# Performance work log

Hardware: AMD Instinct MI355X
Metric: run time of the kernel (lower is better)

Reference implementation:

```python
import jax, jax.numpy as jnp
import numpy as np

# Static hierarchical-sampling layout (hop-sorted prefixes), matching setup_inputs.
C0, C1, C2 = 50_000, 150_000, 300_000   # cumulative node counts for hops 0,1,2
E0, E1 = 300_000, 600_000               # per-edge-type edge counts for hop masks 0,1
T = 3                                    # number of hetero edge types
CIN, HID = 64, 128
LN_EPS = 1e-5
L2_EPS = 1e-12


def _seg_mean(msg, dst, n):
    # PyG scatter-mean: zero for isolated dst nodes
    s = jax.ops.segment_sum(msg, dst, num_segments=n)
    cnt = jax.ops.segment_sum(jnp.ones((dst.shape[0], 1), msg.dtype), dst, num_segments=n)
    return s / jnp.maximum(cnt, 1.0)


def _layer_norm(x, g, b):
    mu = jnp.mean(x, axis=-1, keepdims=True)
    var = jnp.var(x, axis=-1, keepdims=True)
    return (x - mu) * jax.lax.rsqrt(var + LN_EPS) * g + b


def setup_inputs() -> dict:
    key = jax.random.key(0)
    ks = jax.random.split(key, 16)
    x = jax.random.normal(ks[0], (C2, CIN), jnp.float32)
    eis = []
    for t in range(T):
        k1, k2, k3, k4 = jax.random.split(ks[1 + t], 4)
        src0 = jax.random.randint(k1, (E0,), 0, C1, jnp.int32)
        dst0 = jax.random.randint(k2, (E0,), 0, C0, jnp.int32)
        src1 = jax.random.randint(k3, (E1,), 0, C2, jnp.int32)
        dst1 = jax.random.randint(k4, (E1,), 0, C1, jnp.int32)
        eis.append(jnp.stack([jnp.concatenate([src0, src1]),
                              jnp.concatenate([dst0, dst1])]))
    s = 0.05
    Wp = jax.random.normal(ks[4], (T, CIN, CIN), jnp.float32) * s
    bp = jnp.zeros((T, CIN), jnp.float32)
    Wl = jax.random.normal(ks[5], (T, CIN, HID), jnp.float32) * s
    bl = jnp.zeros((T, HID), jnp.float32)
    Wr = jax.random.normal(ks[6], (T, CIN, HID), jnp.float32) * s
    Wl2 = jax.random.normal(ks[7], (T, HID, HID), jnp.float32) * s
    bl2 = jnp.zeros((T, HID), jnp.float32)
    Wr2 = jax.random.normal(ks[8], (T, HID, HID), jnp.float32) * s
    nm_node = jnp.concatenate([jnp.zeros(C0, jnp.int32),
                               jnp.ones(C1 - C0, jnp.int32),
                               jnp.full((C2 - C1,), 2, jnp.int32)])
    nm_edge = jnp.tile(jnp.concatenate([jnp.zeros(E0, jnp.int32),
                                        jnp.ones(E1, jnp.int32)]), T)
    return {"x": x, "ei0": eis[0], "ei1": eis[1], "ei2": eis[2],
            "nm_node": nm_node, "nm_edge": nm_edge,
            "Wp": Wp, "bp": bp, "Wl": Wl, "bl": bl, "Wr": Wr,
            "Wl2": Wl2, "bl2": bl2, "Wr2": Wr2,
            "g0": jnp.ones(HID, jnp.float32), "b0": jnp.zeros(HID, jnp.float32),
            "g1": jnp.ones(HID, jnp.float32), "b1": jnp.zeros(HID, jnp.float32)}


def reference(x, ei0, ei1, ei2, nm_node, nm_edge,
              Wp, bp, Wl, bl, Wr, Wl2, bl2, Wr2, g0, b0, g1, b1):
    eis = (ei0, ei1, ei2)
    # ---- conv 0: SAGEConv(project=True, normalize=True), full graph (trim layer=3) ----
    outs = []
    for t in range(T):
        src, dst = eis[t][0], eis[t][1]
        xp = jax.nn.relu(x @ Wp[t] + bp[t])           # project src features [C2, CIN]
        agg = _seg_mean(xp[src], dst, C2)             # mean over in-neighbors
        o = agg @ Wl[t] + bl[t] + x @ Wr[t]           # lin_l(agg)+bias + lin_r(root)
        o = o / jnp.maximum(jnp.linalg.norm(o, axis=-1, keepdims=True), L2_EPS)
        outs.append(o)
    h = jnp.mean(jnp.stack(outs, 0), 0)               # HeteroConv aggr='mean'
    h = _layer_norm(jax.nn.relu(h), g0, b0)           # relu -> LayerNorm (dropout=eval)
    # ---- conv 1: trim to layer=2 (node prefix C1, hop-0 edges only) ----
    h1 = h[:C1]
    outs = []
    for t in range(T):
        src, dst = eis[t][0, :E0], eis[t][1, :E0]
        agg = _seg_mean(h1[src], dst, C1)
        outs.append(agg @ Wl2[t] + bl2[t] + h1 @ Wr2[t])
    h2 = jnp.mean(jnp.stack(outs, 0), 0)
    h2 = _layer_norm(jax.nn.relu(h2), g1, b1)
    # ---- final trim to layer=1: seed nodes only ----
    return h2[:C0]
```

## Files before the change

### kernel.cpp

```cpp
#include <hip/hip_runtime.h>

#define C0n 50000
#define C1n 150000
#define C2n 300000
#define E0n 300000
#define E1n 600000
#define NEn (E0n + E1n)
#define PAD64 76
#define PAD128 140

typedef float  v4f    __attribute__((ext_vector_type(4)));
typedef float  v2f    __attribute__((ext_vector_type(2)));
typedef float  f32x4  __attribute__((ext_vector_type(4)));
typedef short  bf16x8 __attribute__((ext_vector_type(8)));
typedef unsigned short u16;

__device__ __forceinline__ u16 f2bf(float f){
    unsigned u = __builtin_bit_cast(unsigned, f);
    u += 0x7FFFu + ((u >> 16) & 1u);
    return (u16)(u >> 16);
}
__device__ __forceinline__ float bf2f(u16 h){
    unsigned u = ((unsigned)h) << 16;
    return __builtin_bit_cast(float, u);
}
__device__ __forceinline__ f32x4 mfma16(bf16x8 a, bf16x8 b, f32x4 c){
    return __builtin_amdgcn_mfma_f32_16x16x32_bf16(a, b, c, 0, 0, 0);
}
__device__ __forceinline__ float red16(float v){
    v += __shfl_xor(v, 1); v += __shfl_xor(v, 2);
    v += __shfl_xor(v, 4); v += __shfl_xor(v, 8);
    return v;
}
__device__ __forceinline__ bf16x8 frag8(const float* __restrict__ p){
    v4f a = *(const v4f*)p, b = *(const v4f*)(p + 4);
    bf16x8 r;
    r[0] = (short)f2bf(a[0]); r[1] = (short)f2bf(a[1]);
    r[2] = (short)f2bf(a[2]); r[3] = (short)f2bf(a[3]);
    r[4] = (short)f2bf(b[0]); r[5] = (short)f2bf(b[1]);
    r[6] = (short)f2bf(b[2]); r[7] = (short)f2bf(b[3]);
    return r;
}

__global__ __launch_bounds__(256) void k_wconv(const float* __restrict__ Wp,
    const float* __restrict__ Wl, const float* __restrict__ Wr,
    const float* __restrict__ Wl2, const float* __restrict__ Wr2,
    u16* __restrict__ Wp_c, u16* __restrict__ W1_c, u16* __restrict__ W2_c)
{
    const int i0 = blockIdx.x * 256 + threadIdx.x;
    const int stride = gridDim.x * 256;
    for (int idx = i0; idx < 3 * 64 * PAD64; idx += stride) {
        int t = idx / (64 * PAD64), r = idx % (64 * PAD64);
        int c = r / PAD64, k = r % PAD64;
        Wp_c[idx] = (k < 64) ? f2bf(Wp[t * 4096 + k * 64 + c]) : (u16)0;
    }
    for (int idx = i0; idx < 3 * 128 * PAD128; idx += stride) {
        int t = idx / (128 * PAD128), r = idx % (128 * PAD128);
        int c = r / PAD128, k = r % PAD128;
        u16 v = 0;
        if (k < 64)       v = f2bf(Wl[t * 8192 + k * 128 + c]);
        else if (k < 128) v = f2bf(Wr[t * 8192 + (k - 64) * 128 + c]);
        W1_c[idx] = v;
    }
    for (int idx = i0; idx < 6 * 128 * PAD128; idx += stride) {
        int m = idx / (128 * PAD128), r = idx % (128 * PAD128);
        int t = m % 3;
        const float* W = (m >= 3) ? Wr2 : Wl2;
        int c = r / PAD128, k = r % PAD128;
        W2_c[idx] = (k < 128) ? f2bf(W[t * 16384 + k * 128 + c]) : (u16)0;
    }
}

__global__ __launch_bounds__(256) void k_projm3(const float* __restrict__ x,
    const u16* __restrict__ Wp_c, const float* __restrict__ bp,
    u16* __restrict__ xp3)
{
    __shared__ __align__(16) u16 Wt[3 * 64 * PAD64];
    __shared__ float bps[3 * 64];
    const int tid = threadIdx.x;
    for (int i = tid; i < 192; i += 256) bps[i] = bp[i];
    for (int i = tid; i < 3 * 64 * PAD64 / 8; i += 256)
        ((bf16x8*)Wt)[i] = ((const bf16x8*)Wp_c)[i];
    __syncthreads();

    const int lane = tid & 63, wid = tid >> 6;
    const int lr = lane & 15, lg = lane >> 4;
    const int ntiles = C2n / 16;
    int rt = blockIdx.x * 4 + wid;
    const bool valid = (rt < ntiles);
    if (rt > ntiles - 1) rt = ntiles - 1;
    const int r0 = rt * 16;

    bf16x8 xa[2];
    xa[0] = frag8(&x[(size_t)(r0 + lr) * 64 + 0  + 8 * lg]);
    xa[1] = frag8(&x[(size_t)(r0 + lr) * 64 + 32 + 8 * lg]);

    for (int t = 0; t < 3; t++) {
        f32x4 acc[4];
#pragma unroll
        for (int n = 0; n < 4; n++) acc[n] = 0;
#pragma unroll
        for (int ks = 0; ks < 2; ks++) {
#pragma unroll
            for (int n = 0; n < 4; n++) {
                bf16x8 b = *(const bf16x8*)&Wt[t * 64 * PAD64 + (16 * n + lr) * PAD64 + ks * 32 + 8 * lg];
                acc[n] = mfma16(xa[ks], b, acc[n]);
            }
        }
        if (valid) {
            u16* xp = xp3 + (size_t)t * C2n * 64;
#pragma unroll
            for (int n = 0; n < 4; n++) {
                const float bb = bps[t * 64 + 16 * n + lr];
#pragma unroll
                for (int j = 0; j < 4; j++)
                    xp[(size_t)(r0 + 4 * lg + j) * 64 + 16 * n + lr] =
                        f2bf(fmaxf(acc[n][j] + bb, 0.f));
            }
        }
    }
}

__global__ __launch_bounds__(256) void k_hist(const int* __restrict__ d0,
    const int* __restrict__ d1, const int* __restrict__ d2,
    int* __restrict__ deg, int nE, int nV)
{
    const int e = blockIdx.x * 256 + threadIdx.x;
    if (e >= nE) return;
    const int y = blockIdx.y;
    const int* d = (y == 0) ? d0 : (y == 1) ? d1 : d2;
    atomicAdd(&deg[(size_t)y * nV + d[e]], 1);
}

__global__ __launch_bounds__(256) void k_scan_a(int* __restrict__ a, int n,
    int* __restrict__ bsum, int nblk)
{
    __shared__ int sd[256];
    const int t = threadIdx.x, y = blockIdx.y;
    int* arr = a + (size_t)y * n;
    const int base = blockIdx.x * 2048 + t * 8;
    int v[8];
#pragma unroll
    for (int j = 0; j < 8; j++) v[j] = (base + j < n) ? arr[base + j] : 0;
    int tot = 0;
#pragma unroll
    for (int j = 0; j < 8; j++) { int tmp = v[j]; v[j] = tot; tot += tmp; }
    sd[t] = tot; __syncthreads();
    for (int off = 1; off < 256; off <<= 1) {
        int xv = (t >= off) ? sd[t - off] : 0;
        __syncthreads();
        sd[t] += xv;
        __syncthreads();
    }
    const int excl = sd[t] - tot;
#pragma unroll
    for (int j = 0; j < 8; j++)
        if (base + j < n) arr[base + j] = excl + v[j];
    if (t == 255) bsum[y * nblk + blockIdx.x] = sd[255];
}

__global__ __launch_bounds__(256) void k_scan_b(int* __restrict__ bsum, int nblk)
{
    __shared__ int sd[256];
    const int t = threadIdx.x, y = blockIdx.y;
    int val = (t < nblk) ? bsum[y * nblk + t] : 0;
    sd[t] = val; __syncthreads();
    for (int off = 1; off < 256; off <<= 1) {
        int xv = (t >= off) ? sd[t - off] : 0;
        __syncthreads();
        sd[t] += xv;
        __syncthreads();
    }
    if (t < nblk) bsum[y * nblk + t] = sd[t] - val;
}

__global__ __launch_bounds__(256) void k_scan_c(int* __restrict__ a, int n,
    const int* __restrict__ bsum, int nblk)
{
    const int t = threadIdx.x, y = blockIdx.y;
    int* arr = a + (size_t)y * n;
    const int base = blockIdx.x * 2048 + t * 8;
    const int add = bsum[y * nblk + blockIdx.x];
#pragma unroll
    for (int j = 0; j < 8; j++)
        if (base + j < n) arr[base + j] += add;
}

__global__ __launch_bounds__(256) void k_fill(const int* __restrict__ s0,
    const int* __restrict__ s1, const int* __restrict__ s2,
    const int* __restrict__ d0, const int* __restrict__ d1, const int* __restrict__ d2,
    const int* __restrict__ rp, int* __restrict__ fill, int* __restrict__ el,
    int nE, int nV)
{
    const int e = blockIdx.x * 256 + threadIdx.x;
    if (e >= nE) return;
    const int y = blockIdx.y;
    const int* s = (y == 0) ? s0 : (y == 1) ? s1 : s2;
    const int* d = (y == 0) ? d0 : (y == 1) ? d1 : d2;
    const int dd = d[e];
    const int pos = rp[(size_t)y * nV + dd] + atomicAdd(&fill[(size_t)y * nV + dd], 1);
    el[(size_t)y * nE + pos] = s[e];
}

__global__ __launch_bounds__(256) void k_gath1(const int* __restrict__ rp1,
    const int* __restrict__ el1, const u16* __restrict__ xp3,
    u16* __restrict__ agg3)
{
    const int t = blockIdx.y;
    const int* rp = rp1 + (size_t)t * C1n;
    const int* el = el1 + (size_t)t * NEn;
    const u16* xp = xp3 + (size_t)t * C2n * 64;
    u16* aggt = agg3 + (size_t)t * C1n * 64;

    const int gid = blockIdx.x * 4 + (threadIdx.x >> 6);
    if (gid >= C1n) return;
    const int half = (threadIdx.x >> 5) & 1, l32 = threadIdx.x & 31;
    const int b = rp[gid];
    const int e = (gid == C1n - 1) ? NEn : rp[gid + 1];

    float s0 = 0.f, s1 = 0.f;
    int i = b + half;
    for (; i + 2 < e; i += 4) {
        const int sr0 = el[i], sr1 = el[i + 2];
        unsigned u0 = *(const unsigned*)&xp[(size_t)sr0 * 64 + l32 * 2];
        unsigned u1 = *(const unsigned*)&xp[(size_t)sr1 * 64 + l32 * 2];
        s0 += bf2f((u16)(u0 & 0xffffu)) + bf2f((u16)(u1 & 0xffffu));
        s1 += bf2f((u16)(u0 >> 16)) + bf2f((u16)(u1 >> 16));
    }
    for (; i < e; i += 2) {
        const int sr = el[i];
        unsigned u = *(const unsigned*)&xp[(size_t)sr * 64 + l32 * 2];
        s0 += bf2f((u16)(u & 0xffffu));
        s1 += bf2f((u16)(u >> 16));
    }
    s0 += __shfl_xor(s0, 32);
    s1 += __shfl_xor(s1, 32);
    if (half == 0) {
        const float inv = 1.f / (float)max(e - b, 1);
        unsigned o = (unsigned)f2bf(s0 * inv) | ((unsigned)f2bf(s1 * inv) << 16);
        *(unsigned*)&aggt[(size_t)gid * 64 + l32 * 2] = o;
    }
}

__global__ __launch_bounds__(256) void k_out1f(const u16* __restrict__ agg3,
    const float* __restrict__ x, const u16* __restrict__ W1_c,
    const float* __restrict__ bl,
    const float* __restrict__ g0, const float* __restrict__ b0,
    u16* __restrict__ h1)
{
    __shared__ __align__(16) u16 Wt[128 * PAD128];
    __shared__ float bls[3 * 128], gs[128], bs[128];
    const int tid = threadIdx.x;
    if (tid < 128) { gs[tid] = g0[tid]; bs[tid] = b0[tid]; }
    for (int i = tid; i < 384; i += 256) bls[i] = bl[i];

    const int lane = tid & 63, wid = tid >> 6;
    const int lr = lane & 15, lg = lane >> 4;
    const int ntiles = C1n / 16;
    int rt = blockIdx.x * 4 + wid;
    const bool valid = (rt < ntiles);
    if (rt > ntiles - 1) rt = ntiles - 1;
    const int r0 = rt * 16;

    bf16x8 xa[2];
    xa[0] = frag8(&x[(size_t)(r0 + lr) * 64 + 0  + 8 * lg]);
    xa[1] = frag8(&x[(size_t)(r0 + lr) * 64 + 32 + 8 * lg]);

    f32x4 hacc[8];
#pragma unroll
    for (int n = 0; n < 8; n++) hacc[n] = 0;

    for (int t = 0; t < 3; t++) {
        __syncthreads();
        const bf16x8* src = (const bf16x8*)(W1_c + (size_t)t * 128 * PAD128);
        for (int i = tid; i < 128 * PAD128 / 8; i += 256)
            ((bf16x8*)Wt)[i] = src[i];
        __syncthreads();

        const u16* aggT = agg3 + (size_t)t * C1n * 64;
        f32x4 ta[8];
#pragma unroll
        for (int n = 0; n < 8; n++) ta[n] = 0;
#pragma unroll
        for (int ks = 0; ks < 4; ks++) {
            bf16x8 a;
            if (ks < 2)
                a = *(const bf16x8*)&aggT[(size_t)(r0 + lr) * 64 + ks * 32 + 8 * lg];
            else
                a = xa[ks - 2];
#pragma unroll
            for (int n = 0; n < 8; n++) {
                bf16x8 b = *(const bf16x8*)&Wt[(16 * n + lr) * PAD128 + ks * 32 + 8 * lg];
                ta[n] = mfma16(a, b, ta[n]);
            }
        }
        float ss[4] = {0.f, 0.f, 0.f, 0.f};
#pragma unroll
        for (int n = 0; n < 8; n++) {
            const float bb = bls[t * 128 + 16 * n + lr];
#pragma unroll
            for (int j = 0; j < 4; j++) {
                ta[n][j] += bb;
                ss[j] += ta[n][j] * ta[n][j];
            }
        }
#pragma unroll
        for (int j = 0; j < 4; j++)
            ss[j] = 1.f / fmaxf(sqrtf(red16(ss[j])), 1e-12f);
#pragma unroll
        for (int n = 0; n < 8; n++)
#pragma unroll
            for (int j = 0; j < 4; j++) hacc[n][j] += ta[n][j] * ss[j];
    }

    float mu[4] = {0.f, 0.f, 0.f, 0.f};
#pragma unroll
    for (int n = 0; n < 8; n++)
#pragma unroll
        for (int j = 0; j < 4; j++) {
            float v = fmaxf(hacc[n][j], 0.f) * (1.f / 3.f);
            hacc[n][j] = v; mu[j] += v;
        }
#pragma unroll
    for (int j = 0; j < 4; j++) mu[j] = red16(mu[j]) * (1.f / 128.f);
    float var[4] = {0.f, 0.f, 0.f, 0.f};
#pragma unroll
    for (int n = 0; n < 8; n++)
#pragma unroll
        for (int j = 0; j < 4; j++) {
            float d = hacc[n][j] - mu[j]; var[j] += d * d;
        }
#pragma unroll
    for (int j = 0; j < 4; j++) var[j] = rsqrtf(red16(var[j]) * (1.f / 128.f) + 1e-5f);

    if (valid) {
#pragma unroll
        for (int n = 0; n < 8; n++) {
            const float g = gs[16 * n + lr], bb = bs[16 * n + lr];
#pragma unroll
            for (int j = 0; j < 4; j++) {
                float o = (hacc[n][j] - mu[j]) * var[j] * g + bb;
                h1[(size_t)(r0 + 4 * lg + j) * 128 + 16 * n + lr] = f2bf(o);
            }
        }
    }
}

__global__ __launch_bounds__(256) void k_gath2(const int* __restrict__ rp2,
    const int* __restrict__ el2, const u16* __restrict__ h1,
    u16* __restrict__ agg2)
{
    const int t = blockIdx.y;
    const int* rp = rp2 + (size_t)t * C0n;
    const int* el = el2 + (size_t)t * E0n;
    u16* agg2t = agg2 + (size_t)t * C0n * 128;

    const int gid = blockIdx.x * 4 + (threadIdx.x >> 6);
    if (gid >= C0n) return;
    const int lane = threadIdx.x & 63;
    const int b = rp[gid];
    const int e = (gid == C0n - 1) ? E0n : rp[gid + 1];
    float s0 = 0.f, s1 = 0.f;
    int i = b;
    for (; i + 1 < e; i += 2) {
        const int sr0 = el[i], sr1 = el[i + 1];
        unsigned u0 = *(const unsigned*)&h1[(size_t)sr0 * 128 + lane * 2];
        unsigned u1 = *(const unsigned*)&h1[(size_t)sr1 * 128 + lane * 2];
        s0 += bf2f((u16)(u0 & 0xffffu)) + bf2f((u16)(u1 & 0xffffu));
        s1 += bf2f((u16)(u0 >> 16)) + bf2f((u16)(u1 >> 16));
    }
    if (i < e) {
        const int sr = el[i];
        unsigned u = *(const unsigned*)&h1[(size_t)sr * 128 + lane * 2];
        s0 += bf2f((u16)(u & 0xffffu));
        s1 += bf2f((u16)(u >> 16));
    }
    const float inv = 1.f / (float)max(e - b, 1);
    unsigned o = (unsigned)f2bf(s0 * inv) | ((unsigned)f2bf(s1 * inv) << 16);
    *(unsigned*)&agg2t[(size_t)gid * 128 + lane * 2] = o;
}

__global__ __launch_bounds__(256) void k_out2f(const u16* __restrict__ agg2,
    const u16* __restrict__ h1, const u16* __restrict__ W2_c,
    const float* __restrict__ bl2,
    const float* __restrict__ g1, const float* __restrict__ b1,
    float* __restrict__ out)
{
    __shared__ __align__(16) u16 Wt[128 * PAD128];
    __shared__ float bsm[128], gs[128], bs[128];
    const int tid = threadIdx.x;
    if (tid < 128) {
        gs[tid] = g1[tid]; bs[tid] = b1[tid];
        bsm[tid] = bl2[tid] + bl2[128 + tid] + bl2[256 + tid];
    }
    const int lane = tid & 63, wid = tid >> 6;
    const int lr = lane & 15, lg = lane >> 4;
    const int ntiles = C0n / 16;
    int rt = blockIdx.x * 4 + wid;
    const bool valid = (rt < ntiles);
    if (rt > ntiles - 1) rt = ntiles - 1;
    const int r0 = rt * 16;

    bf16x8 ha[4];
#pragma unroll
    for (int ks = 0; ks < 4; ks++)
        ha[ks] = *(const bf16x8*)&h1[(size_t)(r0 + lr) * 128 + ks * 32 + 8 * lg];

    f32x4 acc[8];
#pragma unroll
    for (int n = 0; n < 8; n++) acc[n] = 0;

    for (int t = 0; t < 3; t++) {
        for (int hh = 0; hh < 2; hh++) {
            __syncthreads();
            const bf16x8* src = (const bf16x8*)(W2_c +
                (size_t)((hh ? 3 : 0) + t) * 128 * PAD128);
            for (int i = tid; i < 128 * PAD128 / 8; i += 256)
                ((bf16x8*)Wt)[i] = src[i];
            __syncthreads();
#pragma unroll
            for (int ks = 0; ks < 4; ks++) {
                bf16x8 a;
                if (hh == 0)
                    a = *(const bf16x8*)&agg2[(size_t)t * C0n * 128 +
                                              (size_t)(r0 + lr) * 128 + ks * 32 + 8 * lg];
                else
                    a = ha[ks];
#pragma unroll
                for (int n = 0; n < 8; n++) {
                    bf16x8 b = *(const bf16x8*)&Wt[(16 * n + lr) * PAD128 + ks * 32 + 8 * lg];
                    acc[n] = mfma16(a, b, acc[n]);
                }
            }
        }
    }

    float mu[4] = {0.f, 0.f, 0.f, 0.f};
#pragma unroll
    for (int n = 0; n < 8; n++) {
        const float bb = bsm[16 * n + lr];
#pragma unroll
        for (int j = 0; j < 4; j++) {
            float v = fmaxf((acc[n][j] + bb) * (1.f / 3.f), 0.f);
            acc[n][j] = v; mu[j] += v;
        }
    }
#pragma unroll
    for (int j = 0; j < 4; j++) mu[j] = red16(mu[j]) * (1.f / 128.f);
    float var[4] = {0.f, 0.f, 0.f, 0.f};
#pragma unroll
    for (int n = 0; n < 8; n++)
#pragma unroll
        for (int j = 0; j < 4; j++) {
            float d = acc[n][j] - mu[j]; var[j] += d * d;
        }
#pragma unroll
    for (int j = 0; j < 4; j++) var[j] = rsqrtf(red16(var[j]) * (1.f / 128.f) + 1e-5f);

    if (valid) {
#pragma unroll
        for (int n = 0; n < 8; n++) {
            const float g = gs[16 * n + lr], bb = bs[16 * n + lr];
#pragma unroll
            for (int j = 0; j < 4; j++) {
                float o = (acc[n][j] - mu[j]) * var[j] * g + bb;
                out[(size_t)(r0 + 4 * lg + j) * 128 + 16 * n + lr] = o;
            }
        }
    }
}

extern "C" void kernel_launch(void* const* d_in, const int* in_sizes, int n_in,
                              void* d_out, int out_size, void* d_ws, size_t ws_size,
                              hipStream_t stream)
{
    const float* x   = (const float*)d_in[0];
    const int*   ei[3] = { (const int*)d_in[1], (const int*)d_in[2], (const int*)d_in[3] };
    const float* Wp  = (const float*)d_in[6];
    const float* bp  = (const float*)d_in[7];
    const float* Wl  = (const float*)d_in[8];
    const float* bl  = (const float*)d_in[9];
    const float* Wr  = (const float*)d_in[10];
    const float* Wl2 = (const float*)d_in[11];
    const float* bl2 = (const float*)d_in[12];
    const float* Wr2 = (const float*)d_in[13];
    const float* g0  = (const float*)d_in[14];
    const float* b0  = (const float*)d_in[15];
    const float* g1  = (const float*)d_in[16];
    const float* b1  = (const float*)d_in[17];

    char* W = (char*)d_ws;
    u16*   agg3 = (u16*)(W + 0);
    u16*   xp3  = (u16*)(W + 57600000);
    u16*   h1   = (u16*)(W + 57600000);
    int*   rp1  = (int*)(W + 172800000);
    int*   fill1= (int*)(W + 174600000);
    int*   bsum = (int*)(W + 176400000);
    int*   el1  = (int*)(W + 176404096);
    u16*   Wp_c = (u16*)(W + 174600000);
    u16*   W1_c = (u16*)(W + 174629184);
    u16*   W2_c = (u16*)(W + 174736704);
    u16*   agg2 = (u16*)(W + 0);
    int*   rp2  = (int*)(W + 38400000);
    int*   fill2= (int*)(W + 39000000);
    int*   el2  = (int*)(W + 39600000);

    const int nb1 = (C1n + 2047) / 2048;
    const int nb2 = (C0n + 2047) / 2048;

    hipMemsetAsync(rp1, 0, 2 * 3 * (size_t)C1n * 4, stream);
    k_hist<<<dim3((NEn + 255) / 256, 3), 256, 0, stream>>>(
        ei[0] + NEn, ei[1] + NEn, ei[2] + NEn, rp1, NEn, C1n);
    k_scan_a<<<dim3(nb1, 3), 256, 0, stream>>>(rp1, C1n, bsum, nb1);
    k_scan_b<<<dim3(1, 3), 256, 0, stream>>>(bsum, nb1);
    k_scan_c<<<dim3(nb1, 3), 256, 0, stream>>>(rp1, C1n, bsum, nb1);
    k_fill<<<dim3((NEn + 255) / 256, 3), 256, 0, stream>>>(
        ei[0], ei[1], ei[2], ei[0] + NEn, ei[1] + NEn, ei[2] + NEn,
        rp1, fill1, el1, NEn, C1n);

    k_wconv<<<176, 256, 0, stream>>>(Wp, Wl, Wr, Wl2, Wr2, Wp_c, W1_c, W2_c);

    k_projm3<<<(C2n / 16 + 3) / 4, 256, 0, stream>>>(x, Wp_c, bp, xp3);
    k_gath1<<<dim3((C1n + 3) / 4, 3), 256, 0, stream>>>(rp1, el1, xp3, agg3);
    k_out1f<<<(C1n / 16 + 3) / 4, 256, 0, stream>>>(agg3, x, W1_c, bl, g0, b0, h1);

    hipMemsetAsync(rp2, 0, 2 * 3 * (size_t)C0n * 4, stream);
    k_hist<<<dim3((E0n + 255) / 256, 3), 256, 0, stream>>>(
        ei[0] + NEn, ei[1] + NEn, ei[2] + NEn, rp2, E0n, C0n);
    k_scan_a<<<dim3(nb2, 3), 256, 0, stream>>>(rp2, C0n, bsum, nb2);
    k_scan_b<<<dim3(1, 3), 256, 0, stream>>>(bsum, nb2);
    k_scan_c<<<dim3(nb2, 3), 256, 0, stream>>>(rp2, C0n, bsum, nb2);
    k_fill<<<dim3((E0n + 255) / 256, 3), 256, 0, stream>>>(
        ei[0], ei[1], ei[2], ei[0] + NEn, ei[1] + NEn, ei[2] + NEn,
        rp2, fill2, el2, E0n, C0n);

    k_gath2<<<dim3((C0n + 3) / 4, 3), 256, 0, stream>>>(rp2, el2, h1, agg2);
    k_out2f<<<(C0n / 16 + 3) / 4, 256, 0, stream>>>(agg2, h1, W2_c, bl2, g1, b1,
                                                    (float*)d_out);
}
```

Measured before the change: 691.3 us.

## Merge both CSR builds into single launches and vectorize gather lanes

The two CSR constructions (hop-0 graph for conv1 and the full graph for conv0) are merged into one set of histogram, scan and fill launches over six edge-type/graph slices. This removes roughly six kernel launches and lets both builds share the GPU at the same time. The gather kernels now give each destination node 16 lanes that do wide 8- or 16-byte loads, instead of a 64-lane wavefront doing 4-byte loads, so more nodes are processed per block with fewer idle lanes on low-degree nodes. The second CSR's buffers are moved to a non-overlapping workspace region, and the gathers drop their bounds checks because the node counts are exact multiples of 16.

Result: faster. 609.1 us (-11.9%).

```diff
diff --git a/kernel.cpp b/kernel.cpp
--- a/kernel.cpp
+++ b/kernel.cpp
@@ -10,7 +10,6 @@
 #define PAD128 140
 
 typedef float  v4f    __attribute__((ext_vector_type(4)));
-typedef float  v2f    __attribute__((ext_vector_type(2)));
 typedef float  f32x4  __attribute__((ext_vector_type(4)));
 typedef short  bf16x8 __attribute__((ext_vector_type(8)));
 typedef unsigned short u16;
@@ -23,6 +22,12 @@
 __device__ __forceinline__ float bf2f(u16 h){
     unsigned u = ((unsigned)h) << 16;
     return __builtin_bit_cast(float, u);
+}
+__device__ __forceinline__ float bf2f_lo(unsigned u){
+    return __builtin_bit_cast(float, u << 16);
+}
+__device__ __forceinline__ float bf2f_hi(unsigned u){
+    return __builtin_bit_cast(float, u & 0xffff0000u);
 }
 __device__ __forceinline__ f32x4 mfma16(bf16x8 a, bf16x8 b, f32x4 c){
     return __builtin_amdgcn_mfma_f32_16x16x32_bf16(a, b, c, 0, 0, 0);
@@ -121,23 +126,27 @@
     }
 }
 
-__global__ __launch_bounds__(256) void k_hist(const int* __restrict__ d0,
+__global__ __launch_bounds__(256) void k_hist6(const int* __restrict__ d0,
     const int* __restrict__ d1, const int* __restrict__ d2,
-    int* __restrict__ deg, int nE, int nV)
+    int* __restrict__ rp1, int* __restrict__ rp2)
 {
     const int e = blockIdx.x * 256 + threadIdx.x;
+    const int y = blockIdx.y;
+    const int g = (y < 3) ? y : y - 3;
+    const int nE = (y < 3) ? NEn : E0n;
     if (e >= nE) return;
-    const int y = blockIdx.y;
-    const int* d = (y == 0) ? d0 : (y == 1) ? d1 : d2;
-    atomicAdd(&deg[(size_t)y * nV + d[e]], 1);
-}
-
-__global__ __launch_bounds__(256) void k_scan_a(int* __restrict__ a, int n,
-    int* __restrict__ bsum, int nblk)
+    const int* d = (g == 0) ? d0 : (g == 1) ? d1 : d2;
+    int* deg = (y < 3) ? rp1 + (size_t)y * C1n : rp2 + (size_t)(y - 3) * C0n;
+    atomicAdd(&deg[d[e]], 1);
+}
+
+__global__ __launch_bounds__(256) void k_scan6_a(int* __restrict__ rp1,
+    int* __restrict__ rp2, int* __restrict__ bsum, int nblk)
 {
     __shared__ int sd[256];
     const int t = threadIdx.x, y = blockIdx.y;
-    int* arr = a + (size_t)y * n;
+    int* arr = (y < 3) ? rp1 + (size_t)y * C1n : rp2 + (size_t)(y - 3) * C0n;
+    const int n = (y < 3) ? C1n : C0n;
     const int base = blockIdx.x * 2048 + t * 8;
     int v[8];
 #pragma unroll
@@ -159,7 +168,7 @@
     if (t == 255) bsum[y * nblk + blockIdx.x] = sd[255];
 }
 
-__global__ __launch_bounds__(256) void k_scan_b(int* __restrict__ bsum, int nblk)
+__global__ __launch_bounds__(256) void k_scan6_b(int* __restrict__ bsum, int nblk)
 {
     __shared__ int sd[256];
     const int t = threadIdx.x, y = blockIdx.y;
@@ -174,11 +183,12 @@
     if (t < nblk) bsum[y * nblk + t] = sd[t] - val;
 }
 
-__global__ __launch_bounds__(256) void k_scan_c(int* __restrict__ a, int n,
-    const int* __restrict__ bsum, int nblk)
+__global__ __launch_bounds__(256) void k_scan6_c(int* __restrict__ rp1,
+    int* __restrict__ rp2, const int* __restrict__ bsum, int nblk)
 {
     const int t = threadIdx.x, y = blockIdx.y;
-    int* arr = a + (size_t)y * n;
+    int* arr = (y < 3) ? rp1 + (size_t)y * C1n : rp2 + (size_t)(y - 3) * C0n;
+    const int n = (y < 3) ? C1n : C0n;
     const int base = blockIdx.x * 2048 + t * 8;
     const int add = bsum[y * nblk + blockIdx.x];
 #pragma unroll
@@ -186,20 +196,26 @@
         if (base + j < n) arr[base + j] += add;
 }
 
-__global__ __launch_bounds__(256) void k_fill(const int* __restrict__ s0,
+__global__ __launch_bounds__(256) void k_fill6(const int* __restrict__ s0,
     const int* __restrict__ s1, const int* __restrict__ s2,
     const int* __restrict__ d0, const int* __restrict__ d1, const int* __restrict__ d2,
-    const int* __restrict__ rp, int* __restrict__ fill, int* __restrict__ el,
-    int nE, int nV)
+    const int* __restrict__ rp1, const int* __restrict__ rp2,
+    int* __restrict__ fill1, int* __restrict__ fill2,
+    int* __restrict__ el1, int* __restrict__ el2)
 {
     const int e = blockIdx.x * 256 + threadIdx.x;
+    const int y = blockIdx.y;
+    const int g = (y < 3) ? y : y - 3;
+    const int nE = (y < 3) ? NEn : E0n;
     if (e >= nE) return;
-    const int y = blockIdx.y;
-    const int* s = (y == 0) ? s0 : (y == 1) ? s1 : s2;
-    const int* d = (y == 0) ? d0 : (y == 1) ? d1 : d2;
+    const int* s = (g == 0) ? s0 : (g == 1) ? s1 : s2;
+    const int* d = (g == 0) ? d0 : (g == 1) ? d1 : d2;
+    const int* rp  = (y < 3) ? rp1  + (size_t)y * C1n : rp2  + (size_t)(y - 3) * C0n;
+    int* fill      = (y < 3) ? fill1 + (size_t)y * C1n : fill2 + (size_t)(y - 3) * C0n;
+    int* el        = (y < 3) ? el1  + (size_t)y * NEn : el2  + (size_t)(y - 3) * E0n;
     const int dd = d[e];
-    const int pos = rp[(size_t)y * nV + dd] + atomicAdd(&fill[(size_t)y * nV + dd], 1);
-    el[(size_t)y * nE + pos] = s[e];
+    const int pos = rp[dd] + atomicAdd(&fill[dd], 1);
+    el[pos] = s[e];
 }
 
 __global__ __launch_bounds__(256) void k_gath1(const int* __restrict__ rp1,
@@ -212,34 +228,32 @@
     const u16* xp = xp3 + (size_t)t * C2n * 64;
     u16* aggt = agg3 + (size_t)t * C1n * 64;
 
-    const int gid = blockIdx.x * 4 + (threadIdx.x >> 6);
-    if (gid >= C1n) return;
-    const int half = (threadIdx.x >> 5) & 1, l32 = threadIdx.x & 31;
+    const int gid = blockIdx.x * 16 + (threadIdx.x >> 4);
+    const int l16 = threadIdx.x & 15;
     const int b = rp[gid];
     const int e = (gid == C1n - 1) ? NEn : rp[gid + 1];
 
-    float s0 = 0.f, s1 = 0.f;
-    int i = b + half;
-    for (; i + 2 < e; i += 4) {
-        const int sr0 = el[i], sr1 = el[i + 2];
-        unsigned u0 = *(const unsigned*)&xp[(size_t)sr0 * 64 + l32 * 2];
-        unsigned u1 = *(const unsigned*)&xp[(size_t)sr1 * 64 + l32 * 2];
-        s0 += bf2f((u16)(u0 & 0xffffu)) + bf2f((u16)(u1 & 0xffffu));
-        s1 += bf2f((u16)(u0 >> 16)) + bf2f((u16)(u1 >> 16));
-    }
-    for (; i < e; i += 2) {
-        const int sr = el[i];
-        unsigned u = *(const unsigned*)&xp[(size_t)sr * 64 + l32 * 2];
-        s0 += bf2f((u16)(u & 0xffffu));
-        s1 += bf2f((u16)(u >> 16));
-    }
-    s0 += __shfl_xor(s0, 32);
-    s1 += __shfl_xor(s1, 32);
-    if (half == 0) {
-        const float inv = 1.f / (float)max(e - b, 1);
-        unsigned o = (unsigned)f2bf(s0 * inv) | ((unsigned)f2bf(s1 * inv) << 16);
-        *(unsigned*)&aggt[(size_t)gid * 64 + l32 * 2] = o;
-    }
+    float s0 = 0.f, s1 = 0.f, s2 = 0.f, s3 = 0.f;
+    int i = b;
+    for (; i + 1 < e; i += 2) {
+        const int sr0 = el[i], sr1 = el[i + 1];
+        uint2 u0 = *(const uint2*)&xp[(size_t)sr0 * 64 + l16 * 4];
+        uint2 u1 = *(const uint2*)&xp[(size_t)sr1 * 64 + l16 * 4];
+        s0 += bf2f_lo(u0.x) + bf2f_lo(u1.x);
+        s1 += bf2f_hi(u0.x) + bf2f_hi(u1.x);
+        s2 += bf2f_lo(u0.y) + bf2f_lo(u1.y);
+        s3 += bf2f_hi(u0.y) + bf2f_hi(u1.y);
+    }
+    if (i < e) {
+        uint2 u = *(const uint2*)&xp[(size_t)el[i] * 64 + l16 * 4];
+        s0 += bf2f_lo(u.x); s1 += bf2f_hi(u.x);
+        s2 += bf2f_lo(u.y); s3 += bf2f_hi(u.y);
+    }
+    const float inv = 1.f / (float)max(e - b, 1);
+    uint2 o;
+    o.x = (unsigned)f2bf(s0 * inv) | ((unsigned)f2bf(s1 * inv) << 16);
+    o.y = (unsigned)f2bf(s2 * inv) | ((unsigned)f2bf(s3 * inv) << 16);
+    *(uint2*)&aggt[(size_t)gid * 64 + l16 * 4] = o;
 }
 
 __global__ __launch_bounds__(256) void k_out1f(const u16* __restrict__ agg3,
@@ -355,29 +369,42 @@
     const int* el = el2 + (size_t)t * E0n;
     u16* agg2t = agg2 + (size_t)t * C0n * 128;
 
-    const int gid = blockIdx.x * 4 + (threadIdx.x >> 6);
-    if (gid >= C0n) return;
-    const int lane = threadIdx.x & 63;
+    const int gid = blockIdx.x * 16 + (threadIdx.x >> 4);
+    const int l16 = threadIdx.x & 15;
     const int b = rp[gid];
     const int e = (gid == C0n - 1) ? E0n : rp[gid + 1];
-    float s0 = 0.f, s1 = 0.f;
+
+    float s[8];
+#pragma unroll
+    for (int j = 0; j < 8; j++) s[j] = 0.f;
     int i = b;
     for (; i + 1 < e; i += 2) {
         const int sr0 = el[i], sr1 = el[i + 1];
-        unsigned u0 = *(const unsigned*)&h1[(size_t)sr0 * 128 + lane * 2];
-        unsigned u1 = *(const unsigned*)&h1[(size_t)sr1 * 128 + lane * 2];
-        s0 += bf2f((u16)(u0 & 0xffffu)) + bf2f((u16)(u1 & 0xffffu));
-        s1 += bf2f((u16)(u0 >> 16)) + bf2f((u16)(u1 >> 16));
+        uint4 u0 = *(const uint4*)&h1[(size_t)sr0 * 128 + l16 * 8];
+        uint4 u1 = *(const uint4*)&h1[(size_t)sr1 * 128 + l16 * 8];
+        s[0] += bf2f_lo(u0.x) + bf2f_lo(u1.x);
+        s[1] += bf2f_hi(u0.x) + bf2f_hi(u1.x);
+        s[2] += bf2f_lo(u0.y) + bf2f_lo(u1.y);
+        s[3] += bf2f_hi(u0.y) + bf2f_hi(u1.y);
+        s[4] += bf2f_lo(u0.z) + bf2f_lo(u1.z);
+        s[5] += bf2f_hi(u0.z) + bf2f_hi(u1.z);
+        s[6] += bf2f_lo(u0.w) + bf2f_lo(u1.w);
+        s[7] += bf2f_hi(u0.w) + bf2f_hi(u1.w);
     }
     if (i < e) {
-        const int sr = el[i];
-        unsigned u = *(const unsigned*)&h1[(size_t)sr * 128 + lane * 2];
-        s0 += bf2f((u16)(u & 0xffffu));
-        s1 += bf2f((u16)(u >> 16));
+        uint4 u = *(const uint4*)&h1[(size_t)el[i] * 128 + l16 * 8];
+        s[0] += bf2f_lo(u.x); s[1] += bf2f_hi(u.x);
+        s[2] += bf2f_lo(u.y); s[3] += bf2f_hi(u.y);
+        s[4] += bf2f_lo(u.z); s[5] += bf2f_hi(u.z);
+        s[6] += bf2f_lo(u.w); s[7] += bf2f_hi(u.w);
     }
     const float inv = 1.f / (float)max(e - b, 1);
-    unsigned o = (unsigned)f2bf(s0 * inv) | ((unsigned)f2bf(s1 * inv) << 16);
-    *(unsigned*)&agg2t[(size_t)gid * 128 + lane * 2] = o;
+    uint4 o;
+    o.x = (unsigned)f2bf(s[0] * inv) | ((unsigned)f2bf(s[1] * inv) << 16);
+    o.y = (unsigned)f2bf(s[2] * inv) | ((unsigned)f2bf(s[3] * inv) << 16);
+    o.z = (unsigned)f2bf(s[4] * inv) | ((unsigned)f2bf(s[5] * inv) << 16);
+    o.w = (unsigned)f2bf(s[6] * inv) | ((unsigned)f2bf(s[7] * inv) << 16);
+    *(uint4*)&agg2t[(size_t)gid * 128 + l16 * 8] = o;
 }
 
 __global__ __launch_bounds__(256) void k_out2f(const u16* __restrict__ agg2,
@@ -497,44 +524,34 @@
     int*   fill1= (int*)(W + 174600000);
     int*   bsum = (int*)(W + 176400000);
     int*   el1  = (int*)(W + 176404096);
+    int*   rp2  = (int*)(W + 187204096);
+    int*   fill2= (int*)(W + 187804096);
+    int*   el2  = (int*)(W + 188404096);
     u16*   Wp_c = (u16*)(W + 174600000);
     u16*   W1_c = (u16*)(W + 174629184);
     u16*   W2_c = (u16*)(W + 174736704);
     u16*   agg2 = (u16*)(W + 0);
-    int*   rp2  = (int*)(W + 38400000);
-    int*   fill2= (int*)(W + 39000000);
-    int*   el2  = (int*)(W + 39600000);
-
-    const int nb1 = (C1n + 2047) / 2048;
-    const int nb2 = (C0n + 2047) / 2048;
+
+    const int nb = (C1n + 2047) / 2048;
 
     hipMemsetAsync(rp1, 0, 2 * 3 * (size_t)C1n * 4, stream);
-    k_hist<<<dim3((NEn + 255) / 256, 3), 256, 0, stream>>>(
-        ei[0] + NEn, ei[1] + NEn, ei[2] + NEn, rp1, NEn, C1n);
-    k_scan_a<<<dim3(nb1, 3), 256, 0, stream>>>(rp1, C1n, bsum, nb1);
-    k_scan_b<<<dim3(1, 3), 256, 0, stream>>>(bsum, nb1);
-    k_scan_c<<<dim3(nb1, 3), 256, 0, stream>>>(rp1, C1n, bsum, nb1);
-    k_fill<<<dim3((NEn + 255) / 256, 3), 256, 0, stream>>>(
+    hipMemsetAsync(rp2, 0, 2 * 3 * (size_t)C0n * 4, stream);
+    k_hist6<<<dim3((NEn + 255) / 256, 6), 256, 0, stream>>>(
+        ei[0] + NEn, ei[1] + NEn, ei[2] + NEn, rp1, rp2);
+    k_scan6_a<<<dim3(nb, 6), 256, 0, stream>>>(rp1, rp2, bsum, nb);
+    k_scan6_b<<<dim3(1, 6), 256, 0, stream>>>(bsum, nb);
+    k_scan6_c<<<dim3(nb, 6), 256, 0, stream>>>(rp1, rp2, bsum, nb);
+    k_fill6<<<dim3((NEn + 255) / 256, 6), 256, 0, stream>>>(
         ei[0], ei[1], ei[2], ei[0] + NEn, ei[1] + NEn, ei[2] + NEn,
-        rp1, fill1, el1, NEn, C1n);
+        rp1, rp2, fill1, fill2, el1, el2);
 
     k_wconv<<<176, 256, 0, stream>>>(Wp, Wl, Wr, Wl2, Wr2, Wp_c, W1_c, W2_c);
 
     k_projm3<<<(C2n / 16 + 3) / 4, 256, 0, stream>>>(x, Wp_c, bp, xp3);
-    k_gath1<<<dim3((C1n + 3) / 4, 3), 256, 0, stream>>>(rp1, el1, xp3, agg3);
+    k_gath1<<<dim3(C1n / 16, 3), 256, 0, stream>>>(rp1, el1, xp3, agg3);
     k_out1f<<<(C1n / 16 + 3) / 4, 256, 0, stream>>>(agg3, x, W1_c, bl, g0, b0, h1);
 
-    hipMemsetAsync(rp2, 0, 2 * 3 * (size_t)C0n * 4, stream);
-    k_hist<<<dim3((E0n + 255) / 256, 3), 256, 0, stream>>>(
-        ei[0] + NEn, ei[1] + NEn, ei[2] + NEn, rp2, E0n, C0n);
-    k_scan_a<<<dim3(nb2, 3), 256, 0, stream>>>(rp2, C0n, bsum, nb2);
-    k_scan_b<<<dim3(1, 3), 256, 0, stream>>>(bsum, nb2);
-    k_scan_c<<<dim3(nb2, 3), 256, 0, stream>>>(rp2, C0n, bsum, nb2);
-    k_fill<<<dim3((E0n + 255) / 256, 3), 256, 0, stream>>>(
-        ei[0], ei[1], ei[2], ei[0] + NEn, ei[1] + NEn, ei[2] + NEn,
-        rp2, fill2, el2, E0n, C0n);
-
-    k_gath2<<<dim3((C0n + 3) / 4, 3), 256, 0, stream>>>(rp2, el2, h1, agg2);
+    k_gath2<<<dim3(C0n / 16, 3), 256, 0, stream>>>(rp2, el2, h1, agg2);
     k_out2f<<<(C0n / 16 + 3) / 4, 256, 0, stream>>>(agg2, h1, W2_c, bl2, g1, b1,
                                                     (float*)d_out);
 }
```
